# Kernel tuning notes

Hardware: AMD Instinct MI355X
Metric: run time of the kernel (lower is better)

The kernel has to match this reference:

```python
import jax, jax.numpy as jnp
import numpy as np

BS, CH, T = 128, 16, 12288
RED = 6          # mini_window_temporal_reduction_factor
N = CH * RED     # 96 mini-windows
K = 5            # top-k selected mini-windows
NCLS = 5
LATENT = (T // 16) * 8  # hypernet flatten dim = 6144


def _conv1d(x, w, b=None):
    # x: [B,C,L], w: [O,I,ks] -> [B,O,L-ks+1]
    out = jax.lax.conv_general_dilated(x, w, (1,), 'VALID', dimension_numbers=('NCH', 'OIH', 'NCH'))
    return out if b is None else out + b[None, :, None]


def _same_reflect(x, w, b):
    p = (w.shape[-1] - 1) // 2
    return _conv1d(jnp.pad(x, ((0, 0), (0, 0), (p, p)), mode='reflect'), w, b)


def _leaky(z):
    return jnp.where(z >= 0, z, 0.01 * z)


def _pool(x, f, op):
    L = x.shape[-1] // f  # floor, drop remainder (matches torch pooling)
    xr = x[..., :L * f].reshape(x.shape[:-1] + (L, f))
    return op(xr, -1)


def setup_inputs() -> dict:
    key = jax.random.key(0)
    ks = jax.random.split(key, 18)
    s = 0.05
    return {
        'x': jax.random.normal(ks[0], (BS, CH, T), jnp.float32),
        'epoch': 0,
        # hypernet conv blocks (padding='same', reflect)
        'hw1': jax.random.normal(ks[1], (32, CH, 7), jnp.float32) * s,
        'hb1': jnp.zeros((32,), jnp.float32),
        'hw2': jax.random.normal(ks[2], (64, 32, 7), jnp.float32) * s,
        'hb2': jnp.zeros((64,), jnp.float32),
        'hw3': jax.random.normal(ks[3], (8, 64, 7), jnp.float32) * s,
        'hb3': jnp.zeros((8,), jnp.float32),
        'hl1': jax.random.normal(ks[4], (N, LATENT), jnp.float32) * s,  # Linear(latent->N), no bias
        'hl2': jax.random.normal(ks[5], (N, N), jnp.float32) * s,       # Linear(N->N), no bias
        # GroupedIdxConv1D: per-group Conv1d(1, 64, ks=15); bias only for group 0
        'gw': jax.random.normal(ks[6], (CH, 64, 15), jnp.float32) * s,
        'gb0': jax.random.normal(ks[7], (64,), jnp.float32) * s,
        # encoder convs 1,2
        'ew2': jax.random.normal(ks[8], (128, 64, 7), jnp.float32) * s,
        'eb2': jnp.zeros((128,), jnp.float32),
        'ew3': jax.random.normal(ks[9], (128, 128, 7), jnp.float32) * s,
        'eb3': jnp.zeros((128,), jnp.float32),
        # classifier
        'cw': jax.random.normal(ks[10], (NCLS, 128), jnp.float32) * s,
        'cb': jnp.zeros((NCLS,), jnp.float32),
    }


def reference(x, epoch, hw1, hb1, hw2, hb2, hw3, hb3, hl1, hl2, gw, gb0, ew2, eb2, ew3, eb3, cw, cb):
    # Eval-mode forward (active sampling, no Gumbel noise, hard top-k one-hot, dropout off)
    bs = x.shape[0]
    # ---- hypernet ----
    h = _pool(_leaky(_same_reflect(x, hw1, hb1)), 4, jnp.mean)
    h = _pool(_leaky(_same_reflect(h, hw2, hb2)), 4, jnp.mean)
    h = jnp.tanh(_same_reflect(h, hw3, hb3)).reshape(bs, -1)
    logits = _leaky(h @ hl1.T) @ hl2.T  # [bs, N]
    # ---- hard top-k sampling (bmm with one-hot == gather rows) ----
    _, idx = jax.lax.top_k(logits, K)                      # [bs, K]
    x_r = x.reshape(bs, N, -1)                             # [bs, N, T']
    sel = jnp.take_along_axis(x_r, idx[:, :, None], axis=1)  # [bs, K, T']
    gidx = idx // RED                                      # ExG channel group per mini-window
    # ---- GroupedIdxConv1D: per-element kernel gather + conv + sum over K ----
    ksz = gw.shape[-1]
    Lout = sel.shape[-1] - ksz + 1
    windows = jnp.stack([sel[..., i:i + Lout] for i in range(ksz)], axis=-1)  # [bs,K,Lout,ksz]
    kernels = gw[gidx]                                     # [bs,K,64,ksz]
    z = jnp.einsum('bkls,bkos->bol', windows, kernels)     # conv + sum over channel axis K
    n0 = (gidx == 0).sum(1).astype(z.dtype)                # bias only for group 0 elements
    z = z + n0[:, None, None] * gb0[None, :, None]
    # ---- encoder tail ----
    z = _pool(_leaky(z), 4, jnp.max)
    z = _pool(_leaky(_conv1d(z, ew2, eb2)), 4, jnp.max)
    z = _conv1d(z, ew3, eb3).mean(-1)                      # AdaptiveAvgPool1d(1) -> [bs,128]
    # ---- classifier ----
    return jax.nn.log_softmax(z @ cw.T + cb, -1)           # [bs, NCLS]
```

## Files before the change

### kernel.cpp

```cpp
#include <hip/hip_runtime.h>
#include <hip/hip_bf16.h>
#include <math.h>

typedef unsigned short u16;
typedef __attribute__((ext_vector_type(8))) short short8;
typedef __attribute__((ext_vector_type(4))) float floatx4;

__device__ __forceinline__ float lk(float v){ return v >= 0.f ? v : 0.01f*v; }
__device__ __forceinline__ u16 f2b(float f){
    __hip_bfloat16 h = __float2bfloat16(f);
    return *reinterpret_cast<u16*>(&h);
}
__device__ __forceinline__ int refl(int t, int L){
    return t < 0 ? -t : (t >= L ? 2*L-2-t : t);
}

__global__ __launch_bounds__(256) void k_prep(const float* __restrict__ hw1,
        const float* __restrict__ hw2, const float* __restrict__ ew2,
        const float* __restrict__ gw, u16* __restrict__ wb)
{
    int idx = blockIdx.x*256 + threadIdx.x;
    if (idx < 4096){
        int u = idx; int j=u&7; int o=(u>>3)&31; int kq=(u>>8)&3; int s=u>>10;
        int tap = 2*s + (kq>>1); int ic = (kq&1)*8 + j;
        wb[idx] = (tap<7) ? f2b(hw1[(o*16+ic)*7+tap]) : (u16)0;
    } else if (idx < 18432){
        int u = idx - 4096; int j=u&7; int o=(u>>3)&63; int kq=(u>>9)&3; int s=u>>11;
        wb[idx] = f2b(hw2[(o*32 + kq*8 + j)*7 + s]);
    } else if (idx < 75776){
        int u = idx - 18432; int j=u&7; int o=(u>>3)&127; int kq=(u>>10)&3; int s=u>>12;
        int ih = s/7, tap = s-ih*7;
        wb[idx] = f2b(ew2[(o*64 + ih*32 + kq*8 + j)*7 + tap]);
    } else if (idx < 92160){
        int u = idx - 75776; int j=u&7; int o=(u>>3)&63; int tb=(u>>9)&1; int gi=u>>10;
        int tap = tb*8 + j;
        wb[idx] = (tap<15) ? f2b(gw[gi*960 + o*15 + tap]) : (u16)0;
    }
}

__global__ __launch_bounds__(256,4) void k_hconv1(const float* __restrict__ x,
        const u16* __restrict__ wb1, const float* __restrict__ bias,
        u16* __restrict__ h1)
{
    __shared__ __align__(16) u16 xs[2][264*24];
    __shared__ __align__(16) u16 ob[2][64*32];
    int b = blockIdx.x >> 3, chunk = blockIdx.x & 7;
    int tid = threadIdx.x;
    const float* xb = x + (size_t)b*16*12288;
    int wv = tid >> 6, lane = tid & 63;
    int m = lane & 15, kq = lane >> 4;
    int tq = wv;

    short8 wfr[4][2];
    #pragma unroll
    for (int s=0;s<4;s++)
        #pragma unroll
        for (int oh=0;oh<2;oh++)
            wfr[s][oh] = *reinterpret_cast<const short8*>(
                            &wb1[(((s*4+kq)*32) + oh*16 + m)*8]);
    float bv[2] = { bias[m], bias[16+m] };

    float rg0[16]; float rgx;
    int exrow = 256 + (tid>>4), exch = tid & 15;

#define LOADTILE(G0) { \
        int t0 = refl((G0) - 3 + tid, 12288); \
        _Pragma("unroll") \
        for (int ic=0;ic<16;ic++) rg0[ic] = xb[(size_t)ic*12288 + t0]; \
        if (tid < 128){ \
            int t1 = refl((G0) - 3 + exrow, 12288); \
            rgx = xb[(size_t)exch*12288 + t1]; \
        } \
        __builtin_amdgcn_sched_barrier(0); }

#define WRITETILE(BUF) { \
        short8 p0, p1; \
        _Pragma("unroll") \
        for (int j=0;j<8;j++){ p0[j] = (short)f2b(rg0[j]); p1[j] = (short)f2b(rg0[8+j]); } \
        *reinterpret_cast<short8*>(&xs[BUF][tid*24])     = p0; \
        *reinterpret_cast<short8*>(&xs[BUF][tid*24 + 8]) = p1; \
        if (tid < 128) xs[BUF][exrow*24 + exch] = f2b(rgx); }

#define COMPUTETILE(BUF) { \
        floatx4 acc[4][2]; \
        _Pragma("unroll") \
        for (int i=0;i<4;i++){ acc[i][0] = (floatx4){0.f,0.f,0.f,0.f}; \
                               acc[i][1] = (floatx4){0.f,0.f,0.f,0.f}; } \
        _Pragma("unroll") \
        for (int sub=0; sub<4; sub++){ \
            int tb = tq*64 + sub*16; \
            _Pragma("unroll") \
            for (int s=0;s<4;s++){ \
                int tap = 2*s + (kq>>1); \
                short8 xfr = *reinterpret_cast<const short8*>( \
                                &xs[BUF][(tb + m + tap)*24 + (kq&1)*8]); \
                acc[sub][0] = __builtin_amdgcn_mfma_f32_16x16x32_bf16(xfr, wfr[s][0], acc[sub][0], 0,0,0); \
                acc[sub][1] = __builtin_amdgcn_mfma_f32_16x16x32_bf16(xfr, wfr[s][1], acc[sub][1], 0,0,0); \
            } \
        } \
        _Pragma("unroll") \
        for (int sub=0; sub<4; sub++){ \
            int p = tq*16 + sub*4 + kq; \
            _Pragma("unroll") \
            for (int oh=0; oh<2; oh++){ \
                float sum = lk(acc[sub][oh][0]+bv[oh]) + lk(acc[sub][oh][1]+bv[oh]) \
                          + lk(acc[sub][oh][2]+bv[oh]) + lk(acc[sub][oh][3]+bv[oh]); \
                ob[BUF][p*32 + oh*16 + m] = f2b(sum*0.25f); \
            } \
        } }

#define STORETILE(BUF, TAU) { \
        short8 v = *reinterpret_cast<const short8*>(&ob[BUF][tid*8]); \
        *reinterpret_cast<short8*>(&h1[((size_t)b*3072 + (TAU)*64)*32 + tid*8]) = v; }

    int tau0 = chunk*6;
    LOADTILE(tau0*256);
    WRITETILE(0);
    __syncthreads();
    LOADTILE((tau0+1)*256);
    #pragma unroll 1
    for (int t=0; t<6; ++t){
        int cur = t & 1;
        COMPUTETILE(cur);
        if (t < 5) WRITETILE(cur^1);
        __syncthreads();
        STORETILE(cur, tau0 + t);
        if (t < 4) LOADTILE((tau0 + t + 2)*256);
    }

#undef LOADTILE
#undef WRITETILE
#undef COMPUTETILE
#undef STORETILE
}

__global__ __launch_bounds__(256,3) void k_hconv2(const u16* __restrict__ h1,
        const u16* __restrict__ wb2, const float* __restrict__ bias,
        float* __restrict__ h2)
{
    __shared__ __align__(16) u16 xs[2][198*40];
    int b = blockIdx.x >> 3, tile = blockIdx.x & 7;
    int tid = threadIdx.x;
    int wv = tid >> 6, lane = tid & 63;
    int m = lane & 15, kq = lane >> 4;

    float bv[4];
    #pragma unroll
    for (int nt=0;nt<4;nt++) bv[nt] = bias[nt*16 + m];

    short8 rgA[3], rgX;

#define LOADH(HALF) { \
        int gh = tile*384 + (HALF)*192 - 3; \
        _Pragma("unroll") \
        for (int cc=0;cc<3;cc++){ \
            int c = tid + cc*256; \
            int row = c >> 2, q = c & 3; \
            int t = refl(gh + row, 3072); \
            rgA[cc] = *reinterpret_cast<const short8*>(&h1[((size_t)b*3072 + t)*32 + q*8]); \
        } \
        if (tid < 24){ \
            int c = 768 + tid; \
            int row = c >> 2, q = c & 3; \
            int t = refl(gh + row, 3072); \
            rgX = *reinterpret_cast<const short8*>(&h1[((size_t)b*3072 + t)*32 + q*8]); \
        } \
        __builtin_amdgcn_sched_barrier(0); }

#define WRITEH(BUF) { \
        _Pragma("unroll") \
        for (int cc=0;cc<3;cc++){ \
            int c = tid + cc*256; \
            *reinterpret_cast<short8*>(&xs[BUF][(c>>2)*40 + (c&3)*8]) = rgA[cc]; \
        } \
        if (tid < 24){ \
            int c = 768 + tid; \
            *reinterpret_cast<short8*>(&xs[BUF][(c>>2)*40 + (c&3)*8]) = rgX; \
        } }

#define COMPUTEH(BUF, HALF) { \
        floatx4 acc[3][4]; \
        _Pragma("unroll") \
        for (int i=0;i<3;i++) \
            _Pragma("unroll") \
            for (int nt=0;nt<4;nt++) acc[i][nt] = (floatx4){0.f,0.f,0.f,0.f}; \
        _Pragma("unroll") \
        for (int nt2=0; nt2<2; ++nt2){ \
            short8 wfr[7][2]; \
            _Pragma("unroll") \
            for (int s=0;s<7;s++) \
                _Pragma("unroll") \
                for (int c=0;c<2;c++) \
                    wfr[s][c] = *reinterpret_cast<const short8*>( \
                        &wb2[(((s*4+kq)*64) + (nt2*2+c)*16 + m)*8]); \
            _Pragma("unroll") \
            for (int i=0;i<3;i++){ \
                int tb = (wv*3+i)*16; \
                _Pragma("unroll") \
                for (int s=0;s<7;s++){ \
                    short8 xfr = *reinterpret_cast<const short8*>( \
                                    &xs[BUF][(tb + m + s)*40 + kq*8]); \
                    acc[i][nt2*2]   = __builtin_amdgcn_mfma_f32_16x16x32_bf16(xfr, wfr[s][0], acc[i][nt2*2],   0,0,0); \
                    acc[i][nt2*2+1] = __builtin_amdgcn_mfma_f32_16x16x32_bf16(xfr, wfr[s][1], acc[i][nt2*2+1], 0,0,0); \
                } \
            } \
        } \
        _Pragma("unroll") \
        for (int i=0;i<3;i++){ \
            int pooled = (wv*3+i)*4 + kq; \
            _Pragma("unroll") \
            for (int nt=0;nt<4;nt++){ \
                float sum = lk(acc[i][nt][0]+bv[nt]) + lk(acc[i][nt][1]+bv[nt]) \
                          + lk(acc[i][nt][2]+bv[nt]) + lk(acc[i][nt][3]+bv[nt]); \
                h2[((size_t)b*768 + tile*96 + (HALF)*48 + pooled)*64 + nt*16 + m] = sum*0.25f; \
            } \
        } }

    LOADH(0);
    WRITEH(0);
    __syncthreads();
    LOADH(1);
    COMPUTEH(0, 0);
    WRITEH(1);
    __syncthreads();
    COMPUTEH(1, 1);

#undef LOADH
#undef WRITEH
#undef COMPUTEH
}

__global__ __launch_bounds__(256) void k_hconv3(const float* __restrict__ h2,
        const float* __restrict__ w, const float* __restrict__ bias,
        float* __restrict__ latent)
{
    __shared__ float xs[64*201];
    int b = blockIdx.x >> 2, tile = blockIdx.x & 3;
    int g0 = tile*192;
    int tid = threadIdx.x;
    for (int idx = tid; idx < 198*64; idx += 256){
        int jj = idx >> 6, ic = idx & 63;
        int t = refl(g0 + jj - 3, 768);
        xs[ic*201 + jj] = h2[((size_t)b*768 + t)*64 + ic];
    }
    __syncthreads();
    int c = tid >> 5, run = tid & 31;
    int p0 = run*6;
    float acc[6];
    #pragma unroll
    for (int l=0;l<6;l++) acc[l] = 0.f;
    for (int ic=0; ic<64; ic++){
        const float* wp = w + (c*64+ic)*7;
        float wr[7];
        #pragma unroll
        for (int s=0;s<7;s++) wr[s] = wp[s];
        const float* xr = xs + ic*201 + p0;
        float xw[12];
        #pragma unroll
        for (int j=0;j<12;j++) xw[j] = xr[j];
        #pragma unroll
        for (int s=0;s<7;s++)
            #pragma unroll
            for (int l=0;l<6;l++) acc[l] += wr[s]*xw[l+s];
    }
    float bv = bias[c];
    float* op = latent + (size_t)b*6144 + c*768 + g0 + p0;
    #pragma unroll
    for (int l=0;l<6;l++) op[l] = tanhf(acc[l] + bv);
}

__global__ __launch_bounds__(256) void k_lin1(const float* __restrict__ latent,
        const float* __restrict__ hl1, float* __restrict__ t1)
{
    __shared__ float ls[6144];
    int b = blockIdx.x / 6, ntile = blockIdx.x % 6;
    int tid = threadIdx.x;
    const float4* lp = reinterpret_cast<const float4*>(latent + (size_t)b*6144);
    float4* lsv = reinterpret_cast<float4*>(ls);
    for (int i = tid; i < 1536; i += 256) lsv[i] = lp[i];
    __syncthreads();
    int wv = tid >> 6, lane = tid & 63;
    #pragma unroll
    for (int nn=0; nn<4; nn++){
        int n = ntile*16 + wv*4 + nn;
        const float4* wp = reinterpret_cast<const float4*>(hl1 + (size_t)n*6144);
        float s = 0.f;
        #pragma unroll
        for (int j=0;j<24;j++){
            float4 q = wp[lane + 64*j];
            float4 l4 = lsv[lane + 64*j];
            s += l4.x*q.x + l4.y*q.y + l4.z*q.z + l4.w*q.w;
        }
        #pragma unroll
        for (int off=32; off; off>>=1) s += __shfl_down(s, off);
        if (lane==0) t1[b*96+n] = lk(s);
    }
}

__global__ __launch_bounds__(128) void k_topk(const float* __restrict__ t1,
        const float* __restrict__ hl2, int* __restrict__ idxb, float* __restrict__ n0f)
{
    __shared__ float lg[96];
    int b = blockIdx.x, n = threadIdx.x;
    if (n < 96){
        float s = 0.f;
        const float* tp = t1 + b*96;
        const float* wp = hl2 + n*96;
        for (int m=0;m<96;m++) s += tp[m]*wp[m];
        lg[n] = s;
    }
    __syncthreads();
    if (threadIdx.x == 0){
        unsigned long long u0=0ull, u1=0ull;
        float n0 = 0.f;
        for (int k=0;k<5;k++){
            float best = -3.4e38f; int bi = 0;
            for (int m=0;m<96;m++){
                bool used = m<64 ? ((u0>>m)&1ull) : ((u1>>(m-64))&1ull);
                if (!used && lg[m] > best){ best = lg[m]; bi = m; }
            }
            if (bi<64) u0 |= 1ull<<bi; else u1 |= 1ull<<(bi-64);
            idxb[b*5+k] = bi;
            if (bi < 6) n0 += 1.f;
        }
        n0f[b] = n0;
    }
}

__global__ __launch_bounds__(256,3) void k_gconv(const float* __restrict__ x,
        const int* __restrict__ idxb, const float* __restrict__ n0f,
        const u16* __restrict__ gwb, const float* __restrict__ gb0,
        u16* __restrict__ zp)
{
    __shared__ __align__(16) u16 xs[5][8][536];
    __shared__ int nidx[5];
    __shared__ float n0s;
    int b = blockIdx.x >> 2, qc = blockIdx.x & 3;
    int tid = threadIdx.x;
    int p0g = qc*512;

    if (tid < 5) nidx[tid] = idxb[b*5 + tid];
    if (tid == 5) n0s = n0f[b];
    __syncthreads();

    for (int cch = tid; cch < 5*134; cch += 256){
        int k = cch / 134, q = cch - k*134;
        const float* xrow = x + (size_t)b*196608 + (size_t)nidx[k]*2048;
        int base = p0g + q*4;
        u16 vb[4];
        if (base + 3 <= 2047){
            float4 a = *reinterpret_cast<const float4*>(xrow + base);
            vb[0]=f2b(a.x); vb[1]=f2b(a.y); vb[2]=f2b(a.z); vb[3]=f2b(a.w);
        } else {
            #pragma unroll
            for (int jj=0;jj<4;jj++){
                int ii = base+jj; if (ii > 2047) ii = 2047;
                vb[jj] = f2b(xrow[ii]);
            }
        }
        #pragma unroll
        for (int jj=0;jj<4;jj++){
            int gof = q*4 + jj;
            #pragma unroll
            for (int r=0;r<8;r++){
                int i = gof - r;
                if (i >= 0 && i < 528) xs[k][r][i] = vb[jj];
            }
        }
    }

    int wv = tid >> 6, lane = tid & 63;
    int m = lane & 15, kq = lane >> 4;
    int o = wv*16 + m;

    short8 wfr[3];
    #pragma unroll
    for (int c=0;c<3;c++){
        int kk = 2*c + (kq>>1);
        int kkc = kk < 5 ? kk : 4;
        int gi = nidx[kkc] / 6;
        short8 f = *reinterpret_cast<const short8*>(
                        &gwb[(((gi*2 + (kq&1))*64)+o)*8]);
        if (kk >= 5) f = (short8)(short)0;
        wfr[c] = f;
    }
    float bv = n0s * gb0[o];
    __syncthreads();

    int rr = m & 7, ibase = (m & 8) + (kq & 1)*8;
    for (int g8 = 0; g8 < 4; ++g8){
        floatx4 acc[8];
        #pragma unroll
        for (int i=0;i<8;i++) acc[i] = (floatx4){0.f,0.f,0.f,0.f};
        #pragma unroll
        for (int s8=0; s8<8; ++s8){
            int P = (g8*8 + s8)*16;
            #pragma unroll
            for (int c=0;c<3;c++){
                int kk = 2*c + (kq>>1);
                int kkc = kk < 5 ? kk : 4;
                short8 af = *reinterpret_cast<const short8*>(&xs[kkc][rr][P + ibase]);
                acc[s8] = __builtin_amdgcn_mfma_f32_16x16x32_bf16(af, wfr[c], acc[s8], 0,0,0);
            }
        }
        #pragma unroll
        for (int s8=0; s8<8; ++s8){
            int sub = g8*8 + s8;
            int Q = qc*128 + sub*4 + kq;
            if (Q < 508){
                float mx = fmaxf(fmaxf(lk(acc[s8][0]+bv), lk(acc[s8][1]+bv)),
                                 fmaxf(lk(acc[s8][2]+bv), lk(acc[s8][3]+bv)));
                zp[((size_t)b*508 + Q)*64 + o] = f2b(mx);
            }
        }
    }
}

__global__ __launch_bounds__(256,2) void k_econv2(const u16* __restrict__ zp,
        const u16* __restrict__ wbe, const float* __restrict__ bias,
        float* __restrict__ p2)
{
    __shared__ __align__(16) u16 xs[118*72];
    int b = blockIdx.x / 5, tile = blockIdx.x % 5;
    int tid = threadIdx.x;
    for (int c = tid; c < 118*8; c += 256){
        int row = c >> 3, q = c & 7;
        int t = tile*100 + row; if (t > 507) t = 507;
        *reinterpret_cast<short8*>(&xs[row*72 + q*8]) =
            *reinterpret_cast<const short8*>(&zp[((size_t)b*508 + t)*64 + q*8]);
    }
    __syncthreads();
    int wv = tid >> 6, lane = tid & 63;
    int m = lane & 15, kq = lane >> 4;
    for (int half=0; half<2; half++){
        int ot = wv + 4*half;
        int o = ot*16 + m;
        short8 wfr[14];
        #pragma unroll
        for (int s=0;s<14;s++)
            wfr[s] = *reinterpret_cast<const short8*>(&wbe[(((s*4+kq)*128)+o)*8]);
        floatx4 acc[7];
        #pragma unroll
        for (int i=0;i<7;i++) acc[i] = (floatx4){0.f,0.f,0.f,0.f};
        #pragma unroll
        for (int sub=0; sub<7; sub++){
            #pragma unroll
            for (int s=0;s<14;s++){
                int tap = s%7, ih = s/7;
                short8 xfr = *reinterpret_cast<const short8*>(
                                &xs[(sub*16 + m + tap)*72 + ih*32 + kq*8]);
                acc[sub] = __builtin_amdgcn_mfma_f32_16x16x32_bf16(xfr, wfr[s], acc[sub], 0,0,0);
            }
        }
        float bv = bias[o];
        #pragma unroll
        for (int sub=0; sub<7; sub++){
            int pidx = sub*4 + kq;
            if (pidx < 25){
                float mx = fmaxf(fmaxf(lk(acc[sub][0]+bv), lk(acc[sub][1]+bv)),
                                 fmaxf(lk(acc[sub][2]+bv), lk(acc[sub][3]+bv)));
                p2[((size_t)b*125 + tile*25 + pidx)*128 + o] = mx;
            }
        }
    }
}

__global__ __launch_bounds__(128) void k_tail(const float* __restrict__ p2,
        const float* __restrict__ w, const float* __restrict__ bias,
        const float* __restrict__ cw, const float* __restrict__ cb,
        float* __restrict__ out)
{
    __shared__ float ss[7][128];
    __shared__ float ft[128];
    __shared__ float lgs[5];
    int b = blockIdx.x, tid = threadIdx.x;

    {
        const float* pb = p2 + (size_t)b*125*128 + tid;
        float first6[6], last6[6];
        float c = 0.f;
        #pragma unroll
        for (int t=0;t<6;t++){ float v = pb[(size_t)t*128]; first6[t]=v; c+=v; }
        for (int t=6;t<119;t++) c += pb[(size_t)t*128];
        #pragma unroll
        for (int t=0;t<6;t++) last6[t] = pb[(size_t)(119+t)*128];
        ss[0][tid] = c;
        #pragma unroll
        for (int s=0;s<6;s++){ c = c - first6[s] + last6[s]; ss[s+1][tid] = c; }
    }
    __syncthreads();

    {
        const float* wp = w + (size_t)tid*896;
        float s = 0.f;
        for (int ic=0; ic<128; ic++){
            #pragma unroll
            for (int tp=0; tp<7; tp++)
                s += wp[ic*7+tp]*ss[tp][ic];
        }
        ft[tid] = s*(1.f/119.f) + bias[tid];
    }
    __syncthreads();

    if (tid < 5){
        float lg = cb[tid];
        const float* wp = cw + tid*128;
        for (int o=0;o<128;o++) lg += ft[o]*wp[o];
        lgs[tid] = lg;
    }
    __syncthreads();
    if (tid == 0){
        float mx = -3.4e38f;
        for (int c=0;c<5;c++) mx = fmaxf(mx, lgs[c]);
        float se = 0.f;
        for (int c=0;c<5;c++) se += expf(lgs[c]-mx);
        float lse = mx + logf(se);
        for (int c=0;c<5;c++) out[b*5+c] = lgs[c]-lse;
    }
}

extern "C" void kernel_launch(void* const* d_in, const int* in_sizes, int n_in,
                              void* d_out, int out_size, void* d_ws, size_t ws_size,
                              hipStream_t stream)
{
    const float* x   = (const float*)d_in[0];
    const float* hw1 = (const float*)d_in[2];
    const float* hb1 = (const float*)d_in[3];
    const float* hw2 = (const float*)d_in[4];
    const float* hb2 = (const float*)d_in[5];
    const float* hw3 = (const float*)d_in[6];
    const float* hb3 = (const float*)d_in[7];
    const float* hl1 = (const float*)d_in[8];
    const float* hl2 = (const float*)d_in[9];
    const float* gw  = (const float*)d_in[10];
    const float* gb0 = (const float*)d_in[11];
    const float* ew2 = (const float*)d_in[12];
    const float* eb2 = (const float*)d_in[13];
    const float* ew3 = (const float*)d_in[14];
    const float* eb3 = (const float*)d_in[15];
    const float* cw  = (const float*)d_in[16];
    const float* cb  = (const float*)d_in[17];
    float* out = (float*)d_out;

    float* f       = (float*)d_ws;
    float* latent  = f;
    float* t1      = f + 786432;
    int*   idxb    = (int*)(f + 806432);
    float* n0f     = f + 808432;
    u16*   zpb     = (u16*)(f + 810000);
    u16*   wb      = (u16*)(f + 2900000);
    float* h2      = f + 3932160;
    float* p2      = f + 5000000;
    u16*   h1b     = (u16*)(f + 10223616);

    k_prep<<<360, 256, 0, stream>>>(hw1, hw2, ew2, gw, wb);
    k_hconv1<<<1024, 256, 0, stream>>>(x, wb, hb1, h1b);
    k_hconv2<<<1024, 256, 0, stream>>>(h1b, wb + 4096, hb2, h2);
    k_hconv3<<<512, 256, 0, stream>>>(h2, hw3, hb3, latent);
    k_lin1<<<768, 256, 0, stream>>>(latent, hl1, t1);
    k_topk<<<128, 128, 0, stream>>>(t1, hl2, idxb, n0f);
    k_gconv<<<512, 256, 0, stream>>>(x, idxb, n0f, wb + 75776, gb0, zpb);
    k_econv2<<<640, 256, 0, stream>>>(zpb, wb + 18432, eb2, p2);
    k_tail<<<128, 128, 0, stream>>>(p2, ew3, eb3, cw, cb, out);
}
```

Before: 421.7 us.

## Enlarge econv2 tiles to two per batch and reuse each input fragment across two output tiles

The encoder conv2 kernel now covers each batch with two large time tiles instead of five small ones, which cuts the halo rows reloaded per block. Each wave keeps weight fragments for two output-channel tiles in registers and applies every loaded input fragment to both, halving LDS reads per MFMA. The weight loads now run before the barrier, overlapping the shared-memory fill. In exchange the grid drops to 256 blocks, exactly the CU count, and launch bounds allow only one block per CU, so occupancy and latency hiding fall.

```diff
diff --git a/kernel.cpp b/kernel.cpp
--- a/kernel.cpp
+++ b/kernel.cpp
@@ -416,50 +416,54 @@
     }
 }
 
-__global__ __launch_bounds__(256,2) void k_econv2(const u16* __restrict__ zp,
+__global__ __launch_bounds__(256,1) void k_econv2(const u16* __restrict__ zp,
         const u16* __restrict__ wbe, const float* __restrict__ bias,
         float* __restrict__ p2)
 {
-    __shared__ __align__(16) u16 xs[118*72];
-    int b = blockIdx.x / 5, tile = blockIdx.x % 5;
+    __shared__ __align__(16) u16 xs[262*72];
+    int b = blockIdx.x >> 1, tile = blockIdx.x & 1;
     int tid = threadIdx.x;
-    for (int c = tid; c < 118*8; c += 256){
+    int r0 = tile*252;
+    for (int c = tid; c < 262*8; c += 256){
         int row = c >> 3, q = c & 7;
-        int t = tile*100 + row; if (t > 507) t = 507;
+        int t = r0 + row; if (t > 505) t = 505;
         *reinterpret_cast<short8*>(&xs[row*72 + q*8]) =
             *reinterpret_cast<const short8*>(&zp[((size_t)b*508 + t)*64 + q*8]);
     }
-    __syncthreads();
     int wv = tid >> 6, lane = tid & 63;
     int m = lane & 15, kq = lane >> 4;
-    for (int half=0; half<2; half++){
-        int ot = wv + 4*half;
-        int o = ot*16 + m;
-        short8 wfr[14];
+    int npool = tile ? 62 : 63;
+
+    short8 wfr[2][14];
+    #pragma unroll
+    for (int h=0;h<2;h++){
+        int o = (wv + 4*h)*16 + m;
         #pragma unroll
         for (int s=0;s<14;s++)
-            wfr[s] = *reinterpret_cast<const short8*>(&wbe[(((s*4+kq)*128)+o)*8]);
-        floatx4 acc[7];
-        #pragma unroll
-        for (int i=0;i<7;i++) acc[i] = (floatx4){0.f,0.f,0.f,0.f};
-        #pragma unroll
-        for (int sub=0; sub<7; sub++){
+            wfr[h][s] = *reinterpret_cast<const short8*>(&wbe[(((s*4+kq)*128)+o)*8]);
+    }
+    float bv[2] = { bias[wv*16 + m], bias[(wv+4)*16 + m] };
+    __syncthreads();
+
+    for (int sub=0; sub<16; sub++){
+        floatx4 acc[2];
+        acc[0] = (floatx4){0.f,0.f,0.f,0.f};
+        acc[1] = (floatx4){0.f,0.f,0.f,0.f};
+        #pragma unroll
+        for (int s=0;s<14;s++){
+            int tap = s%7, ih = s/7;
+            short8 xfr = *reinterpret_cast<const short8*>(
+                            &xs[(sub*16 + m + tap)*72 + ih*32 + kq*8]);
+            acc[0] = __builtin_amdgcn_mfma_f32_16x16x32_bf16(xfr, wfr[0][s], acc[0], 0,0,0);
+            acc[1] = __builtin_amdgcn_mfma_f32_16x16x32_bf16(xfr, wfr[1][s], acc[1], 0,0,0);
+        }
+        int pidx = sub*4 + kq;
+        if (pidx < npool){
             #pragma unroll
-            for (int s=0;s<14;s++){
-                int tap = s%7, ih = s/7;
-                short8 xfr = *reinterpret_cast<const short8*>(
-                                &xs[(sub*16 + m + tap)*72 + ih*32 + kq*8]);
-                acc[sub] = __builtin_amdgcn_mfma_f32_16x16x32_bf16(xfr, wfr[s], acc[sub], 0,0,0);
-            }
-        }
-        float bv = bias[o];
-        #pragma unroll
-        for (int sub=0; sub<7; sub++){
-            int pidx = sub*4 + kq;
-            if (pidx < 25){
-                float mx = fmaxf(fmaxf(lk(acc[sub][0]+bv), lk(acc[sub][1]+bv)),
-                                 fmaxf(lk(acc[sub][2]+bv), lk(acc[sub][3]+bv)));
-                p2[((size_t)b*125 + tile*25 + pidx)*128 + o] = mx;
+            for (int h=0;h<2;h++){
+                float mx = fmaxf(fmaxf(lk(acc[h][0]+bv[h]), lk(acc[h][1]+bv[h])),
+                                 fmaxf(lk(acc[h][2]+bv[h]), lk(acc[h][3]+bv[h])));
+                p2[((size_t)b*125 + tile*63 + pidx)*128 + (wv+4*h)*16 + m] = mx;
             }
         }
     }
@@ -560,6 +564,6 @@
     k_lin1<<<768, 256, 0, stream>>>(latent, hl1, t1);
     k_topk<<<128, 128, 0, stream>>>(t1, hl2, idxb, n0f);
     k_gconv<<<512, 256, 0, stream>>>(x, idxb, n0f, wb + 75776, gb0, zpb);
-    k_econv2<<<640, 256, 0, stream>>>(zpb, wb + 18432, eb2, p2);
+    k_econv2<<<256, 256, 0, stream>>>(zpb, wb + 18432, eb2, p2);
     k_tail<<<128, 128, 0, stream>>>(p2, ew3, eb3, cw, cb, out);
 }
```

Result: faster. 350.7 us (-16.8%).
